# Kernel optimization log

Hardware: AMD Instinct MI355X
Metric: run time of the kernel (lower is better)

Reference implementation:

```python
import jax, jax.numpy as jnp
import numpy as np

N = 100000
E = 1600000
DIN = 256
DOUT = 64


def setup_inputs() -> dict:
    key = jax.random.key(0)
    ks = jax.random.split(key, 12)
    s = 1.0 / np.sqrt(DIN)
    so = 1.0 / np.sqrt(DOUT)
    return {
        "x": jax.random.normal(ks[0], (N, DIN), dtype=jnp.float32),
        "edge_index": jax.random.randint(ks[1], (2, E), 0, N, dtype=jnp.int32),
        "W_hp": jax.random.uniform(ks[2], (DIN, DOUT), jnp.float32, -s, s),
        "b_hp": jnp.zeros((DOUT,), jnp.float32),
        "W_lp": jax.random.uniform(ks[3], (DIN, DOUT), jnp.float32, -s, s),
        "b_lp": jnp.zeros((DOUT,), jnp.float32),
        "W_i": jax.random.uniform(ks[4], (DIN, DOUT), jnp.float32, -s, s),
        "b_i": jnp.zeros((DOUT,), jnp.float32),
        "w_h": jax.random.uniform(ks[5], (DOUT, 1), jnp.float32, -so, so),
        "b_h": jnp.zeros((1,), jnp.float32),
        "w_l": jax.random.uniform(ks[6], (DOUT, 1), jnp.float32, -so, so),
        "b_l": jnp.zeros((1,), jnp.float32),
        "w_i2": jax.random.uniform(ks[7], (DOUT, 1), jnp.float32, -so, so),
        "b_i2": jnp.zeros((1,), jnp.float32),
    }


def _gcn_norm(edge_index, n):
    # add self loops, symmetric GCN normalization
    ar = jnp.arange(n, dtype=edge_index.dtype)
    src = jnp.concatenate([edge_index[0], ar])
    dst = jnp.concatenate([edge_index[1], ar])
    deg = jax.ops.segment_sum(jnp.ones_like(dst, dtype=jnp.float32), dst, num_segments=n)
    dinv = jnp.where(deg > 0, jax.lax.rsqrt(jnp.maximum(deg, 1e-12)), 0.0)
    norm = dinv[src] * dinv[dst]  # [E+N]
    return src, dst, norm


def reference(x, edge_index, W_hp, b_hp, W_lp, b_lp, W_i, b_i,
              w_h, b_h, w_l, b_l, w_i2, b_i2):
    n = x.shape[0]
    src, dst, norm = _gcn_norm(edge_index, n)

    def prop(h):  # Ahat @ h via gather-scale-scatter
        return jax.ops.segment_sum(h[src] * norm[:, None], dst, num_segments=n)

    # three ACM-GCN filter branches
    xw_hp = x @ W_hp + b_hp
    H_hp = jax.nn.relu(xw_hp - prop(xw_hp))      # high-pass: (I - Ahat) X W
    H_lp = jax.nn.relu(prop(x @ W_lp + b_lp))    # low-pass:  Ahat X W
    H_i = jax.nn.relu(x @ W_i + b_i)             # identity:  X W

    # per-node sigmoid gates (mix=False path)
    a_h = jax.nn.sigmoid(H_hp @ w_h + b_h)[:, 0]
    a_l = jax.nn.sigmoid(H_lp @ w_l + b_l)[:, 0]
    a_i = jax.nn.sigmoid(H_i @ w_i2 + b_i2)[:, 0]

    # diag(alpha) @ H == broadcasted row scaling (same math, no NxN diag)
    out = a_h[:, None] * H_hp + a_l[:, None] * H_lp + a_i[:, None] * H_i
    return jax.nn.log_softmax(out, axis=1)
```

## Files before the change

### kernel.cpp

```cpp
#include <hip/hip_runtime.h>
#include <hip/hip_bf16.h>
#include <hip/hip_fp16.h>
#include <math.h>

#define DIN 256
#define DOUT 64

#define BKT_CAP 1408
#define C1_CAP 36864
#define CH1 4096
#define CH2 4096
#define NB2_PER 9

typedef __attribute__((ext_vector_type(8))) short bfrag8;
typedef __attribute__((ext_vector_type(4))) float ffrag4;
typedef __fp16 fp16x2 __attribute__((ext_vector_type(2)));

#define AS1 __attribute__((address_space(1)))
#define AS3 __attribute__((address_space(3)))

__device__ inline unsigned short f2bf(float f) {
    union { float f; unsigned u; } v; v.f = f;
    unsigned r = v.u + 0x7FFF + ((v.u >> 16) & 1);
    return (unsigned short)(r >> 16);
}
__device__ inline unsigned cvt2(float a, float b) {
    unsigned r;
    asm("v_cvt_pk_bf16_f32 %0, %1, %2" : "=v"(r) : "v"(a), "v"(b));
    return r;
}

__device__ inline float wave_sum(float v) {
    #pragma unroll
    for (int off = 32; off > 0; off >>= 1) v += __shfl_xor(v, off, 64);
    return v;
}
__device__ inline float wave_max(float v) {
    #pragma unroll
    for (int off = 32; off > 0; off >>= 1) v = fmaxf(v, __shfl_xor(v, off, 64));
    return v;
}

__device__ inline void gload16(const void* g, void* l) {
    __builtin_amdgcn_global_load_lds((const AS1 void*)g, (AS3 void*)l, 16, 0, 0);
}

union HU { unsigned u; __half2 h; };

__device__ inline void prew_body(int id, const float* __restrict__ Whp,
                                 const float* __restrict__ Wlp,
                                 const float* __restrict__ Wi,
                                 unsigned* __restrict__ wt) {
    if (id >= 8 * 192 * 4) return;
    int p = id & 3;
    int col = (id >> 2) % 192;
    int kci = id / (192 * 4);
    int s = p ^ ((col >> 1) & 3);
    int m = col >> 6, c = col & 63;
    const float* W = (m == 0) ? Whp : ((m == 1) ? Wlp : Wi);
    int k0 = kci * 32 + s * 4;
    unsigned o0 = (unsigned)f2bf(W[(k0 + 0) * 64 + c]) | ((unsigned)f2bf(W[(k0 + 1) * 64 + c]) << 16);
    unsigned o1 = (unsigned)f2bf(W[(k0 + 2) * 64 + c]) | ((unsigned)f2bf(W[(k0 + 3) * 64 + c]) << 16);
    unsigned o2 = (unsigned)f2bf(W[(k0 + 16) * 64 + c]) | ((unsigned)f2bf(W[(k0 + 17) * 64 + c]) << 16);
    unsigned o3 = (unsigned)f2bf(W[(k0 + 18) * 64 + c]) | ((unsigned)f2bf(W[(k0 + 19) * 64 + c]) << 16);
    uint4 v; v.x = o0; v.y = o1; v.z = o2; v.w = o3;
    *(uint4*)&wt[(size_t)id * 4] = v;
}

__global__ __launch_bounds__(256) void k_bin1(
    const int* __restrict__ src, const int* __restrict__ dst, int E,
    int* __restrict__ gcnt1, unsigned* __restrict__ cwords,
    const float* __restrict__ Whp, const float* __restrict__ Wlp,
    const float* __restrict__ Wi, unsigned* __restrict__ wt) {
    __shared__ int hist[64], loff[64], gb[64];
    __shared__ unsigned words[CH1];
    __shared__ unsigned char aux[CH1];
    int t = threadIdx.x;
    int base = blockIdx.x * CH1;
    int nloc = E - base;
    if (nloc > CH1) nloc = CH1;
    if (nloc < 0) nloc = 0;
    if (t < 64) hist[t] = 0;
    __syncthreads();
    unsigned myw[16];
    short myr[16];
    signed char myb[16];
    #pragma unroll
    for (int i = 0; i < 16; ++i) {
        int idx = i * 256 + t;
        myb[i] = -1;
        if (idx < nloc) {
            int s = src[base + idx], d = dst[base + idx];
            int b = d >> 11;
            myw[i] = (unsigned)s | ((unsigned)(d & 2047) << 17);
            myb[i] = (signed char)b;
            myr[i] = (short)atomicAdd(&hist[b], 1);
        }
    }
    __syncthreads();
    if (t == 0) {
        int run = 0;
        for (int i2 = 0; i2 < 64; ++i2) { loff[i2] = run; run += hist[i2]; }
    }
    __syncthreads();
    if (t < 64) {
        int c = hist[t];
        gb[t] = c ? atomicAdd(&gcnt1[t], c) : 0;
    }
    __syncthreads();
    #pragma unroll
    for (int i = 0; i < 16; ++i) {
        if (myb[i] >= 0) {
            int pos = loff[myb[i]] + myr[i];
            words[pos] = myw[i];
            aux[pos] = (unsigned char)myb[i];
        }
    }
    __syncthreads();
    for (int j = t; j < nloc; j += 256) {
        int b = aux[j];
        int g = gb[b] + (j - loff[b]);
        if (g < C1_CAP) cwords[(size_t)b * C1_CAP + g] = words[j];
    }
    if (blockIdx.x < 24) prew_body(blockIdx.x * 256 + t, Whp, Wlp, Wi, wt);
}

__global__ __launch_bounds__(256) void k_bin2(
    const int* __restrict__ gcnt1, const unsigned* __restrict__ cwords,
    int* __restrict__ gcnt2, unsigned* __restrict__ bwords,
    int* __restrict__ cnt, int N) {
    __shared__ int hist[32], loff[32], gb[32];
    __shared__ int hist2k[2048];
    __shared__ unsigned words[CH2];
    __shared__ unsigned char aux[CH2];
    int t = threadIdx.x;
    int b = blockIdx.x / NB2_PER, j = blockIdx.x % NB2_PER;
    int tot = gcnt1[b];
    if (tot > C1_CAP) tot = C1_CAP;
    int base = j * CH2;
    int nloc = tot - base;
    if (nloc <= 0) return;
    if (nloc > CH2) nloc = CH2;
    if (t < 32) hist[t] = 0;
    for (int i = t; i < 2048; i += 256) hist2k[i] = 0;
    __syncthreads();
    unsigned myw[16];
    short myr[16];
    signed char myf[16];
    const unsigned* cw = cwords + (size_t)b * C1_CAP + base;
    #pragma unroll
    for (int i = 0; i < 16; ++i) {
        int idx = i * 256 + t;
        myf[i] = -1;
        if (idx < nloc) {
            unsigned w = cw[idx];
            int ld = (int)(w >> 17);
            int f = ld >> 6;
            myw[i] = (w & 0x1FFFF) | ((unsigned)(ld & 63) << 17);
            myf[i] = (signed char)f;
            myr[i] = (short)atomicAdd(&hist[f], 1);
            atomicAdd(&hist2k[ld], 1);
        }
    }
    __syncthreads();
    if (t == 0) {
        int run = 0;
        for (int i2 = 0; i2 < 32; ++i2) { loff[i2] = run; run += hist[i2]; }
    }
    __syncthreads();
    if (t < 32) {
        int c = hist[t];
        gb[t] = c ? atomicAdd(&gcnt2[b * 32 + t], c) : 0;
    }
    __syncthreads();
    #pragma unroll
    for (int i = 0; i < 16; ++i) {
        if (myf[i] >= 0) {
            int pos = loff[myf[i]] + myr[i];
            words[pos] = myw[i];
            aux[pos] = (unsigned char)myf[i];
        }
    }
    __syncthreads();
    for (int j2 = t; j2 < nloc; j2 += 256) {
        int f = aux[j2];
        int g = gb[f] + (j2 - loff[f]);
        if (g < BKT_CAP) bwords[(size_t)(b * 32 + f) * BKT_CAP + g] = words[j2];
    }
    int nbase = b * 2048;
    for (int i = t; i < 2048; i += 256) {
        int c = hist2k[i];
        if (c && nbase + i < N) atomicAdd(&cnt[nbase + i], c);
    }
}

__global__ __launch_bounds__(256) void k_gemm(
    const float* __restrict__ x, int N,
    const unsigned* __restrict__ wt,
    const float* __restrict__ bhp, const float* __restrict__ blp,
    const float* __restrict__ bi, const int* __restrict__ cnt,
    unsigned* __restrict__ xws, __half* __restrict__ xwi) {
    __shared__ __attribute__((aligned(16))) float Al[2][128 * 32];
    __shared__ __attribute__((aligned(16))) unsigned short Bl[2][192 * 32];
    int t = threadIdx.x;
    int wave = t >> 6, lane = t & 63;
    int l15 = lane & 15, lhi = lane >> 4;
    int row0 = blockIdx.x * 128;

    ffrag4 acc[2][12];
    #pragma unroll
    for (int mf = 0; mf < 2; ++mf)
        #pragma unroll
        for (int nf = 0; nf < 12; ++nf)
            acc[mf][nf] = (ffrag4){0.f, 0.f, 0.f, 0.f};

    int arow[4], achk[4];
    #pragma unroll
    for (int i = 0; i < 4; ++i) {
        int off = i * 4096 + t * 16;
        int r = off >> 7;
        int cp = (off >> 4) & 7;
        arow[i] = row0 + r < N ? row0 + r : N - 1;
        achk[i] = cp ^ (r & 7);
    }

    auto stage = [&](int buf, int kci) {
        #pragma unroll
        for (int i = 0; i < 4; ++i)
            gload16(x + (size_t)arow[i] * DIN + kci * 32 + achk[i] * 4,
                    (char*)Al[buf] + i * 4096 + wave * 1024);
        #pragma unroll
        for (int i = 0; i < 3; ++i)
            gload16(wt + (size_t)kci * 3072 + ((i * 4096 + t * 16) >> 2),
                    (char*)Bl[buf] + i * 4096 + wave * 1024);
    };

    stage(0, 0);
    __syncthreads();
    for (int kci = 0; kci < 8; ++kci) {
        int cur = kci & 1;
        if (kci < 7) stage(cur ^ 1, kci + 1);

        union { bfrag8 v; unsigned u[4]; } af[2];
        #pragma unroll
        for (int mf = 0; mf < 2; ++mf) {
            int row = wave * 32 + mf * 16 + l15;
            int p1 = lhi ^ (row & 7);
            float4 lo = ((const float4*)Al[cur])[row * 8 + p1];
            float4 hi = ((const float4*)Al[cur])[row * 8 + (p1 ^ 4)];
            af[mf].u[0] = cvt2(lo.x, lo.y);
            af[mf].u[1] = cvt2(lo.z, lo.w);
            af[mf].u[2] = cvt2(hi.x, hi.y);
            af[mf].u[3] = cvt2(hi.z, hi.w);
        }
        bfrag8 bfr[12];
        #pragma unroll
        for (int nf = 0; nf < 12; ++nf) {
            int col = nf * 16 + l15;
            int p = lhi ^ ((col >> 1) & 3);
            bfr[nf] = *((const bfrag8*)Bl[cur] + col * 4 + p);
        }
        #pragma unroll
        for (int mf = 0; mf < 2; ++mf)
            #pragma unroll
            for (int nf = 0; nf < 12; ++nf)
                acc[mf][nf] = __builtin_amdgcn_mfma_f32_16x16x32_bf16(
                    af[mf].v, bfr[nf], acc[mf][nf], 0, 0, 0);
        __syncthreads();
    }

    #pragma unroll
    for (int mf = 0; mf < 2; ++mf) {
        #pragma unroll
        for (int nf = 0; nf < 4; ++nf) {
            int col = nf * 16 + l15;
            float bh_ = bhp[col], bl_ = blp[col], bi_ = bi[col];
            #pragma unroll
            for (int r = 0; r < 4; ++r) {
                int grow = row0 + wave * 32 + mf * 16 + lhi * 4 + r;
                if (grow >= N) continue;
                float dv = rsqrtf((float)cnt[grow] + 1.f);
                float hp = (acc[mf][nf][r] + bh_) * dv;
                float lp = (acc[mf][nf + 4][r] + bl_) * dv;
                union { fp16x2 p; unsigned u; } pu;
                pu.p = __builtin_amdgcn_cvt_pkrtz(hp, lp);
                xws[(size_t)grow * 64 + col] = pu.u;
                xwi[(size_t)grow * 64 + col] = __float2half(acc[mf][nf + 8][r] + bi_);
            }
        }
    }
}

__global__ __launch_bounds__(256) void k_bagg(
    const int* __restrict__ gcnt2, const unsigned* __restrict__ bwords,
    const unsigned* __restrict__ xws, const __half* __restrict__ xwi,
    const float* __restrict__ wh, const float* __restrict__ bh,
    const float* __restrict__ wl, const float* __restrict__ bl,
    const float* __restrict__ wi2, const float* __restrict__ bi2,
    float* __restrict__ out, int N) {
    __shared__ unsigned sorted[1024];
    __shared__ int h2[32], lo2[32], sc[32];
    int t = threadIdx.x, bb = blockIdx.x;
    int b = bb >> 1, half = bb & 1;
    int n0 = b * 64 + half * 32;
    if (n0 >= N) return;
    int cntE = gcnt2[b];
    if (cntE > BKT_CAP) cntE = BKT_CAP;
    if (t < 32) h2[t] = 0;
    __syncthreads();
    unsigned mw[6];
    short ml[6], mr[6];
    #pragma unroll
    for (int i = 0; i < 6; ++i) {
        int idx = i * 256 + t;
        ml[i] = -1;
        if (idx < cntE) {
            unsigned w = bwords[(size_t)b * BKT_CAP + idx];
            int ld = (int)(w >> 17);
            if ((ld >> 5) == half) {
                int l5 = ld & 31;
                mw[i] = (w & 0x1FFFF) << 8;
                ml[i] = (short)l5;
                mr[i] = (short)atomicAdd(&h2[l5], 1);
            }
        }
    }
    __syncthreads();
    if (t < 32) sc[t] = h2[t];
    __syncthreads();
    for (int off = 1; off < 32; off <<= 1) {
        int x = (t < 32 && t >= off) ? sc[t - off] : 0;
        __syncthreads();
        if (t < 32) sc[t] += x;
        __syncthreads();
    }
    if (t < 32) lo2[t] = sc[t] - h2[t];
    __syncthreads();
    #pragma unroll
    for (int i = 0; i < 6; ++i)
        if (ml[i] >= 0) {
            int pos = lo2[ml[i]] + mr[i];
            if (pos < 1024) sorted[pos] = mw[i];
        }
    __syncthreads();

    int wave = t >> 6, lane = t & 63;
    int h = lane >> 5, f2 = lane & 31;
    const unsigned laneoff = (unsigned)(f2 * 8);
    const char* bp = (const char*)xws;
    float wh0 = wh[f2 * 2], wh1 = wh[f2 * 2 + 1];
    float wl0 = wl[f2 * 2], wl1 = wl[f2 * 2 + 1];
    float wi0 = wi2[f2 * 2], wi1 = wi2[f2 * 2 + 1];
    float bhv = bh[0], blv = bl[0], biv = bi2[0];
    for (int ni = 0; ni < 8; ++ni) {
        int ln = wave * 8 + ni;
        int node = n0 + ln;
        if (node >= N) break;
        int c = h2[ln], e0 = lo2[ln], e1 = e0 + c;
        if (e1 > 1024) e1 = 1024;
        unsigned long long us = *(const unsigned long long*)(bp + ((unsigned)node << 8) + laneoff);
        HU z; z.u = 0;
        __half2 acc0 = z.h, acc1 = z.h;
        int e = e0;
        for (; e + 16 <= e1; e += 16) {
            unsigned long long v[8];
            #pragma unroll
            for (int k = 0; k < 8; ++k)
                v[k] = *(const unsigned long long*)(bp + (sorted[e + 2 * k + h] + laneoff));
            #pragma unroll
            for (int k = 0; k < 8; ++k) {
                HU a, bq;
                a.u = (unsigned)v[k];
                bq.u = (unsigned)(v[k] >> 32);
                acc0 = __hadd2(acc0, a.h);
                acc1 = __hadd2(acc1, bq.h);
            }
        }
        if (e + 8 <= e1) {
            unsigned long long v[4];
            #pragma unroll
            for (int k = 0; k < 4; ++k)
                v[k] = *(const unsigned long long*)(bp + (sorted[e + 2 * k + h] + laneoff));
            #pragma unroll
            for (int k = 0; k < 4; ++k) {
                HU a, bq;
                a.u = (unsigned)v[k];
                bq.u = (unsigned)(v[k] >> 32);
                acc0 = __hadd2(acc0, a.h);
                acc1 = __hadd2(acc1, bq.h);
            }
            e += 8;
        }
        if (e + 4 <= e1) {
            unsigned long long v[2];
            #pragma unroll
            for (int k = 0; k < 2; ++k)
                v[k] = *(const unsigned long long*)(bp + (sorted[e + 2 * k + h] + laneoff));
            #pragma unroll
            for (int k = 0; k < 2; ++k) {
                HU a, bq;
                a.u = (unsigned)v[k];
                bq.u = (unsigned)(v[k] >> 32);
                acc0 = __hadd2(acc0, a.h);
                acc1 = __hadd2(acc1, bq.h);
            }
            e += 4;
        }
        for (; e < e1; e += 2) {
            int ei = e + h;
            if (ei < e1) {
                unsigned long long v = *(const unsigned long long*)(bp + (sorted[ei] + laneoff));
                HU a, bq;
                a.u = (unsigned)v;
                bq.u = (unsigned)(v >> 32);
                acc0 = __hadd2(acc0, a.h);
                acc1 = __hadd2(acc1, bq.h);
            }
        }
        HU c0, c1;
        c0.h = acc0; c0.u = __shfl_xor(c0.u, 32, 64);
        c1.h = acc1; c1.u = __shfl_xor(c1.u, 32, 64);
        acc0 = __hadd2(acc0, c0.h);
        acc1 = __hadd2(acc1, c1.h);
        float s_h0 = __low2float(acc0), s_l0 = __high2float(acc0);
        float s_h1 = __low2float(acc1), s_l1 = __high2float(acc1);
        float fc = (float)c + 1.f;
        float dv = rsqrtf(fc), sq = sqrtf(fc);
        HU q0, q1;
        q0.u = (unsigned)us; q1.u = (unsigned)(us >> 32);
        float xh0 = __low2float(q0.h), xl0 = __high2float(q0.h);
        float xh1 = __low2float(q1.h), xl1 = __high2float(q1.h);
        float Hh0 = fmaxf(xh0 * sq - dv * (s_h0 + xh0), 0.f);
        float Hh1 = fmaxf(xh1 * sq - dv * (s_h1 + xh1), 0.f);
        float Hl0 = fmaxf(dv * (s_l0 + xl0), 0.f);
        float Hl1 = fmaxf(dv * (s_l1 + xl1), 0.f);
        HU qi;
        qi.u = *(const unsigned*)((const char*)xwi + ((size_t)node * 128) + f2 * 4);
        float Hi0 = fmaxf(__low2float(qi.h), 0.f);
        float Hi1 = fmaxf(__high2float(qi.h), 0.f);
        float zh = 0.5f * wave_sum(Hh0 * wh0 + Hh1 * wh1) + bhv;
        float zl = 0.5f * wave_sum(Hl0 * wl0 + Hl1 * wl1) + blv;
        float zi = 0.5f * wave_sum(Hi0 * wi0 + Hi1 * wi1) + biv;
        float ah = 1.f / (1.f + expf(-zh));
        float al = 1.f / (1.f + expf(-zl));
        float ai = 1.f / (1.f + expf(-zi));
        float o0 = ah * Hh0 + al * Hl0 + ai * Hi0;
        float o1 = ah * Hh1 + al * Hl1 + ai * Hi1;
        float mx = wave_max(fmaxf(o0, o1));
        float ss = 0.5f * wave_sum(expf(o0 - mx) + expf(o1 - mx));
        float lse = mx + logf(ss);
        if (h == 0) {
            float2 r; r.x = o0 - lse; r.y = o1 - lse;
            *(float2*)&out[(size_t)node * 64 + f2 * 2] = r;
        }
    }
}

extern "C" void kernel_launch(void* const* d_in, const int* in_sizes, int n_in,
                              void* d_out, int out_size, void* d_ws, size_t ws_size,
                              hipStream_t stream) {
    const float* x   = (const float*)d_in[0];
    const int*   ei  = (const int*)d_in[1];
    const float* Whp = (const float*)d_in[2];
    const float* bhp = (const float*)d_in[3];
    const float* Wlp = (const float*)d_in[4];
    const float* blp = (const float*)d_in[5];
    const float* Wi  = (const float*)d_in[6];
    const float* bi  = (const float*)d_in[7];
    const float* wh  = (const float*)d_in[8];
    const float* bh  = (const float*)d_in[9];
    const float* wl  = (const float*)d_in[10];
    const float* bl  = (const float*)d_in[11];
    const float* wi2 = (const float*)d_in[12];
    const float* bi2 = (const float*)d_in[13];
    float* out = (float*)d_out;

    int N = in_sizes[0] / DIN;
    int E = in_sizes[1] / 2;
    const int* src = ei;
    const int* dst = ei + E;
    int nc = (N + 2047) >> 11;
    int nbuck2 = nc * 32;

    char* w = (char*)d_ws;
    size_t off = 0;
    auto alloc = [&](size_t bytes) {
        void* p = w + off;
        off += (bytes + 255) & ~size_t(255);
        return p;
    };
    int*      cnt    = (int*)alloc((size_t)N * 4);
    int*      gcnt1  = (int*)alloc(64 * 4);
    int*      gcnt2  = (int*)alloc((size_t)nbuck2 * 4);
    size_t    zero_end = off;
    unsigned* cwords = (unsigned*)alloc((size_t)nc * C1_CAP * 4);
    unsigned* bwords = (unsigned*)alloc((size_t)nbuck2 * BKT_CAP * 4);
    unsigned* xws    = (unsigned*)alloc((size_t)N * 64 * 4);
    __half*   xwi    = (__half*)alloc((size_t)N * 64 * 2);
    unsigned* wt     = (unsigned*)alloc((size_t)8 * 192 * 4 * 16);
    (void)ws_size; (void)n_in; (void)out_size;

    hipError_t e0 = hipMemsetAsync(cnt, 0, zero_end, stream); (void)e0;
    k_bin1<<<(E + CH1 - 1) / CH1, 256, 0, stream>>>(src, dst, E, gcnt1, cwords,
                                                    Whp, Wlp, Wi, wt);
    k_bin2<<<nc * NB2_PER, 256, 0, stream>>>(gcnt1, cwords, gcnt2, bwords, cnt, N);
    k_gemm<<<(N + 127) / 128, 256, 0, stream>>>(x, N, wt, bhp, blp, bi, cnt,
                                                xws, xwi);
    k_bagg<<<nbuck2 * 2, 256, 0, stream>>>(gcnt2, bwords, xws, xwi,
                                           wh, bh, wl, bl, wi2, bi2, out, N);
}
```

Measured before the change: 150.6 us.

## Replicate bin1 histogram per lane group and single-buffer GEMM LDS tiles

In the edge-binning kernel, the shared histogram is split into four replicas indexed by thread id mod 4, with per-replica offsets, to reduce LDS atomic contention on hot buckets. In the GEMM kernel, the double-buffered A/B LDS tiles become single buffers loaded and then synchronized each k-step. This halves shared memory use so more blocks can be resident, but it gives up overlap of the next tile's global loads with the current MFMA work.

```diff
diff --git a/kernel.cpp b/kernel.cpp
--- a/kernel.cpp
+++ b/kernel.cpp
@@ -72,15 +72,18 @@
     int* __restrict__ gcnt1, unsigned* __restrict__ cwords,
     const float* __restrict__ Whp, const float* __restrict__ Wlp,
     const float* __restrict__ Wi, unsigned* __restrict__ wt) {
-    __shared__ int hist[64], loff[64], gb[64];
+    __shared__ int hist[4][64];
+    __shared__ int roff[4][64];
+    __shared__ int loff[64], gb[64];
     __shared__ unsigned words[CH1];
     __shared__ unsigned char aux[CH1];
     int t = threadIdx.x;
+    int rep = t & 3;
     int base = blockIdx.x * CH1;
     int nloc = E - base;
     if (nloc > CH1) nloc = CH1;
     if (nloc < 0) nloc = 0;
-    if (t < 64) hist[t] = 0;
+    if (t < 64) { hist[0][t] = 0; hist[1][t] = 0; hist[2][t] = 0; hist[3][t] = 0; }
     __syncthreads();
     unsigned myw[16];
     short myr[16];
@@ -94,26 +97,34 @@
             int b = d >> 11;
             myw[i] = (unsigned)s | ((unsigned)(d & 2047) << 17);
             myb[i] = (signed char)b;
-            myr[i] = (short)atomicAdd(&hist[b], 1);
-        }
+            myr[i] = (short)atomicAdd(&hist[rep][b], 1);
+        }
+    }
+    __syncthreads();
+    if (t < 64) {
+        int run = 0;
+        #pragma unroll
+        for (int r = 0; r < 4; ++r) { roff[r][t] = run; run += hist[r][t]; }
+        hist[0][t] = run;
     }
     __syncthreads();
     if (t == 0) {
         int run = 0;
-        for (int i2 = 0; i2 < 64; ++i2) { loff[i2] = run; run += hist[i2]; }
+        for (int i2 = 0; i2 < 64; ++i2) { loff[i2] = run; run += hist[0][i2]; }
     }
     __syncthreads();
     if (t < 64) {
-        int c = hist[t];
+        int c = hist[0][t];
         gb[t] = c ? atomicAdd(&gcnt1[t], c) : 0;
     }
     __syncthreads();
     #pragma unroll
     for (int i = 0; i < 16; ++i) {
         if (myb[i] >= 0) {
-            int pos = loff[myb[i]] + myr[i];
+            int b = myb[i];
+            int pos = loff[b] + roff[rep][b] + myr[i];
             words[pos] = myw[i];
-            aux[pos] = (unsigned char)myb[i];
+            aux[pos] = (unsigned char)b;
         }
     }
     __syncthreads();
@@ -200,8 +211,8 @@
     const float* __restrict__ bhp, const float* __restrict__ blp,
     const float* __restrict__ bi, const int* __restrict__ cnt,
     unsigned* __restrict__ xws, __half* __restrict__ xwi) {
-    __shared__ __attribute__((aligned(16))) float Al[2][128 * 32];
-    __shared__ __attribute__((aligned(16))) unsigned short Bl[2][192 * 32];
+    __shared__ __attribute__((aligned(16))) float Al[128 * 32];
+    __shared__ __attribute__((aligned(16))) unsigned short Bl[192 * 32];
     int t = threadIdx.x;
     int wave = t >> 6, lane = t & 63;
     int l15 = lane & 15, lhi = lane >> 4;
@@ -224,30 +235,24 @@
         achk[i] = cp ^ (r & 7);
     }
 
-    auto stage = [&](int buf, int kci) {
+    for (int kci = 0; kci < 8; ++kci) {
         #pragma unroll
         for (int i = 0; i < 4; ++i)
             gload16(x + (size_t)arow[i] * DIN + kci * 32 + achk[i] * 4,
-                    (char*)Al[buf] + i * 4096 + wave * 1024);
+                    (char*)Al + i * 4096 + wave * 1024);
         #pragma unroll
         for (int i = 0; i < 3; ++i)
             gload16(wt + (size_t)kci * 3072 + ((i * 4096 + t * 16) >> 2),
-                    (char*)Bl[buf] + i * 4096 + wave * 1024);
-    };
-
-    stage(0, 0);
-    __syncthreads();
-    for (int kci = 0; kci < 8; ++kci) {
-        int cur = kci & 1;
-        if (kci < 7) stage(cur ^ 1, kci + 1);
+                    (char*)Bl + i * 4096 + wave * 1024);
+        __syncthreads();
 
         union { bfrag8 v; unsigned u[4]; } af[2];
         #pragma unroll
         for (int mf = 0; mf < 2; ++mf) {
             int row = wave * 32 + mf * 16 + l15;
             int p1 = lhi ^ (row & 7);
-            float4 lo = ((const float4*)Al[cur])[row * 8 + p1];
-            float4 hi = ((const float4*)Al[cur])[row * 8 + (p1 ^ 4)];
+            float4 lo = ((const float4*)Al)[row * 8 + p1];
+            float4 hi = ((const float4*)Al)[row * 8 + (p1 ^ 4)];
             af[mf].u[0] = cvt2(lo.x, lo.y);
             af[mf].u[1] = cvt2(lo.z, lo.w);
             af[mf].u[2] = cvt2(hi.x, hi.y);
@@ -258,7 +263,7 @@
         for (int nf = 0; nf < 12; ++nf) {
             int col = nf * 16 + l15;
             int p = lhi ^ ((col >> 1) & 3);
-            bfr[nf] = *((const bfrag8*)Bl[cur] + col * 4 + p);
+            bfr[nf] = *((const bfrag8*)Bl + col * 4 + p);
         }
         #pragma unroll
         for (int mf = 0; mf < 2; ++mf)
```

Result: no change. 147.8 us, median of 2 (-1.9%).
